# Optimization experiments

Measured on AMD Instinct MI355X. Metric: run time of the kernel, lower is better.

Reference implementation:

```python
import jax, jax.numpy as jnp
import numpy as np

B, PATCH, S, D, LAYERS, TOP_K, N_HEADS = 32, 196, 77, 512, 2, 16, 8


def setup_inputs() -> dict:
    key = jax.random.key(0)
    ks = jax.random.split(key, 16)
    d, L = D, LAYERS
    attn_std = d ** -0.5
    proj_std = (d ** -0.5) * ((2 * L) ** -0.5)
    fc_std = (2 * d) ** -0.5
    scale = d ** -0.5
    f = jnp.float32
    return {
        'image_feature': jax.random.normal(ks[0], (B, d), f),
        'image_tokens': jax.random.normal(ks[1], (B, PATCH, d), f),
        'text_feature': jax.random.normal(ks[2], (B, d), f),
        'text_tokens': jax.random.normal(ks[3], (B, S, d), f),
        'atte_mask': jax.random.randint(ks[4], (B, S), 0, 2).astype(jnp.int32),
        'img_cls': scale * jax.random.normal(ks[5], (d,), f),
        'txt_cls': scale * jax.random.normal(ks[6], (d,), f),
        'in_proj_w': attn_std * jax.random.normal(ks[7], (L, 3 * d, d), f),
        'in_proj_b': jnp.zeros((L, 3 * d), f),
        'out_w': proj_std * jax.random.normal(ks[8], (L, d, d), f),
        'out_b': jnp.zeros((L, d), f),
        'ln1_w': jnp.ones((L, d), f), 'ln1_b': jnp.zeros((L, d), f),
        'ln2_w': jnp.ones((L, d), f), 'ln2_b': jnp.zeros((L, d), f),
        'ln3_w': jnp.ones((L, d), f), 'ln3_b': jnp.zeros((L, d), f),
        'fc_w': fc_std * jax.random.normal(ks[9], (L, 4 * d, d), f),
        'fc_b': jnp.zeros((L, 4 * d), f),
        'proj_w': proj_std * jax.random.normal(ks[10], (L, d, 4 * d), f),
        'proj_b': jnp.zeros((L, d), f),
    }


def _ln(x, w, b):
    m = jnp.mean(x, axis=-1, keepdims=True)
    v = jnp.mean((x - m) ** 2, axis=-1, keepdims=True)
    return (x - m) * jax.lax.rsqrt(v + 1e-5) * w + b


def _mha(q, k, wi, bi, wo, bo):
    # q: (N, Lq, d), k: (N, Lk, d)
    N, Lq, d = q.shape
    hd = d // N_HEADS
    qh = (q @ wi[:d].T + bi[:d]).reshape(N, Lq, N_HEADS, hd)
    kh = (k @ wi[d:2 * d].T + bi[d:2 * d]).reshape(N, -1, N_HEADS, hd)
    vh = (k @ wi[2 * d:].T + bi[2 * d:]).reshape(N, -1, N_HEADS, hd)
    att = jax.nn.softmax(jnp.einsum('bqhd,bkhd->bhqk', qh, kh) * (hd ** -0.5), axis=-1)
    o = jnp.einsum('bhqk,bkhd->bqhd', att, vh).reshape(N, Lq, d)
    return o @ wo.T + bo


def _cross_attention(q4, k4, p):
    shape4 = q4.shape
    q = q4.reshape(-1, q4.shape[-2], q4.shape[-1])
    k = k4.reshape(-1, k4.shape[-2], k4.shape[-1])
    for i in range(LAYERS):
        kn = _ln(k, p['ln2_w'][i], p['ln2_b'][i])
        q = q + _mha(_ln(q, p['ln1_w'][i], p['ln1_b'][i]), kn,
                     p['in_proj_w'][i], p['in_proj_b'][i], p['out_w'][i], p['out_b'][i])
        h = _ln(q, p['ln3_w'][i], p['ln3_b'][i]) @ p['fc_w'][i].T + p['fc_b'][i]
        h = h * jax.nn.sigmoid(1.702 * h)  # QuickGELU
        q = q + h @ p['proj_w'][i].T + p['proj_b'][i]
    return q.reshape(shape4)


def _forward(image_feature, image_tokens, text_feature, text_tokens, atte_mask,
             img_cls, txt_cls, p):
    b, patch, d = image_tokens.shape
    s = text_tokens.shape[1]
    img_n = image_tokens / jnp.linalg.norm(image_tokens, axis=-1, keepdims=True)
    txt_n = text_tokens / jnp.linalg.norm(text_tokens, axis=-1, keepdims=True)
    # pairwise token similarities: (b_img, b_txt, patch, s)
    sim = jnp.einsum('ipd,jsd->ijps', img_n, txt_n)
    img_scores = jnp.einsum('ijps,js->ijp', sim, atte_mask.astype(sim.dtype))
    txt_scores = sim.sum(axis=2)  # (b, b, s)
    # top-k; torch scatter+masked_select gathers in ascending index order
    idx_i = jnp.sort(jax.lax.top_k(img_scores, TOP_K)[1], axis=-1)  # (b,b,k)
    idx_t = jnp.sort(jax.lax.top_k(txt_scores, TOP_K)[1], axis=-1)
    img_sel = img_n[jnp.arange(b)[:, None, None], idx_i]  # (b,b,k,d)
    txt_sel = txt_n[jnp.arange(b)[None, :, None], idx_t]  # (b,b,k,d)
    img_feat = jnp.broadcast_to(image_feature[:, None, None, :], (b, b, 1, d))
    txt_feat = jnp.broadcast_to(text_feature[None, :, None, :], (b, b, 1, d))
    img_cls4 = jnp.broadcast_to(img_cls, (b, b, 1, d))
    txt_cls4 = jnp.broadcast_to(txt_cls, (b, b, 1, d))
    final_img = _cross_attention(jnp.concatenate([img_cls4, img_sel], axis=2),
                                 jnp.concatenate([txt_feat, txt_sel], axis=2), p)
    final_txt = _cross_attention(jnp.concatenate([txt_cls4, txt_sel], axis=2),
                                 jnp.concatenate([img_feat, img_sel], axis=2), p)
    return final_img, final_txt


def reference(image_feature, image_tokens, text_feature, text_tokens, atte_mask,
              img_cls, txt_cls, in_proj_w, in_proj_b, out_w, out_b,
              ln1_w, ln1_b, ln2_w, ln2_b, ln3_w, ln3_b,
              fc_w, fc_b, proj_w, proj_b):
    p = dict(in_proj_w=in_proj_w, in_proj_b=in_proj_b, out_w=out_w, out_b=out_b,
             ln1_w=ln1_w, ln1_b=ln1_b, ln2_w=ln2_w, ln2_b=ln2_b,
             ln3_w=ln3_w, ln3_b=ln3_b, fc_w=fc_w, fc_b=fc_b,
             proj_w=proj_w, proj_b=proj_b)
    return _forward(image_feature, image_tokens, text_feature, text_tokens,
                    atte_mask, img_cls, txt_cls, p)
```

## Files before the change

### kernel.cpp

```cpp
#include <hip/hip_runtime.h>
#include <hip/hip_bf16.h>
#include <stdint.h>


typedef __attribute__((ext_vector_type(8))) short short8;
typedef __attribute__((ext_vector_type(4))) float f32x4;

__device__ __forceinline__ float bf2f(short u) {
    return __uint_as_float(((uint32_t)(uint16_t)u) << 16);
}
__device__ __forceinline__ unsigned short f2bf(float f) {
    __hip_bfloat16 h = __float2bfloat16(f);
    return *reinterpret_cast<unsigned short*>(&h);
}
__device__ __forceinline__ void gload16(const void* g, void* l) {
    __builtin_amdgcn_global_load_lds(
        (const __attribute__((address_space(1))) unsigned int*)g,
        (__attribute__((address_space(3))) unsigned int*)l, 16, 0, 0);
}

__global__ __launch_bounds__(256) void k_f2b4(const float* __restrict__ s0,
                                              const float* __restrict__ s1,
                                              const float* __restrict__ s2,
                                              const float* __restrict__ s3,
                                              unsigned short* __restrict__ out) {
    for (int i = blockIdx.x * 256 + threadIdx.x; i < 6291456; i += gridDim.x * 256) {
        float v;
        if (i < 1572864) v = s0[i];
        else if (i < 2097152) v = s1[i - 1572864];
        else if (i < 4194304) v = s2[i - 2097152];
        else v = s3[i - 4194304];
        out[i] = f2bf(v);
    }
}

__global__ __launch_bounds__(256) void k_l2norm(const float* __restrict__ in,
                                                float* __restrict__ out) {
    size_t row = blockIdx.x;
    const float* x = in + row * 512;
    int t = threadIdx.x;
    float a0 = x[t], a1 = x[t + 256];
    float ss = a0 * a0 + a1 * a1;
#pragma unroll
    for (int off = 32; off; off >>= 1) ss += __shfl_xor(ss, off);
    __shared__ float s4[4];
    if ((t & 63) == 0) s4[t >> 6] = ss;
    __syncthreads();
    float tot = s4[0] + s4[1] + s4[2] + s4[3];
    float inv = 1.0f / sqrtf(tot);
    out[row * 512 + t] = a0 * inv;
    out[row * 512 + t + 256] = a1 * inv;
}

__global__ __launch_bounds__(512) void k_colsum(const float* __restrict__ tok,
                                                const int* __restrict__ mask,
                                                float* __restrict__ out, int R) {
    int b = blockIdx.x;
    int d = threadIdx.x;
    float acc = 0.f;
    for (int r = 0; r < R; r++) {
        float m = mask ? (float)mask[b * R + r] : 1.f;
        acc += m * tok[((size_t)b * R + r) * 512 + d];
    }
    out[b * 512 + d] = acc;
}

__global__ __launch_bounds__(256) void k_scores(const float* __restrict__ tok,
                                                const float* __restrict__ vec,
                                                float* __restrict__ out, int R, int swap) {
    int bid = blockIdx.x;
    int i = bid >> 5, j = bid & 31;
    int tb = swap ? j : i;
    int vb = swap ? i : j;
    __shared__ float sv[512];
    for (int t = threadIdx.x; t < 512; t += 256) sv[t] = vec[vb * 512 + t];
    __syncthreads();
    int wv = threadIdx.x >> 6, lane = threadIdx.x & 63;
    for (int r = wv; r < R; r += 4) {
        const float* tr = tok + ((size_t)tb * R + r) * 512;
        float acc = 0.f;
#pragma unroll
        for (int c = 0; c < 8; c++) {
            int d = lane + c * 64;
            acc += tr[d] * sv[d];
        }
#pragma unroll
        for (int off = 32; off; off >>= 1) acc += __shfl_xor(acc, off);
        if (lane == 0) out[(size_t)bid * R + r] = acc;
    }
}

__global__ __launch_bounds__(64) void k_topk(const float* __restrict__ simg,
                                             const float* __restrict__ stxt,
                                             int* __restrict__ idx_i, int* __restrict__ idx_t) {
    int bid = blockIdx.x;
    bool isimg = bid < 1024;
    int ij = isimg ? bid : bid - 1024;
    const float* s = isimg ? simg + (size_t)ij * 196 : stxt + (size_t)ij * 77;
    int n = isimg ? 196 : 77;
    int* out = (isimg ? idx_i : idx_t) + ij * 16;
    int lane = threadIdx.x;
    float v[4];
    int ids[4];
#pragma unroll
    for (int k = 0; k < 4; k++) {
        int id = lane + k * 64;
        ids[k] = id;
        v[k] = (id < n) ? s[id] : -3.0e38f;
    }
    __shared__ int sel[16];
    for (int r = 0; r < 16; r++) {
        float bv = v[0];
        int bi = ids[0];
#pragma unroll
        for (int k = 1; k < 4; k++)
            if (v[k] > bv) { bv = v[k]; bi = ids[k]; }
#pragma unroll
        for (int off = 32; off; off >>= 1) {
            float ov = __shfl_xor(bv, off);
            int oi = __shfl_xor(bi, off);
            if (ov > bv || (ov == bv && oi < bi)) { bv = ov; bi = oi; }
        }
        if (lane == 0) sel[r] = bi;
#pragma unroll
        for (int k = 0; k < 4; k++)
            if (ids[k] == bi) v[k] = -3.0e38f;
    }
    if (lane == 0) {
        for (int a = 1; a < 16; a++) {
            int key = sel[a];
            int b = a - 1;
            while (b >= 0 && sel[b] > key) { sel[b + 1] = sel[b]; b--; }
            sel[b + 1] = key;
        }
        for (int a = 0; a < 16; a++) out[a] = sel[a];
    }
}

__global__ __launch_bounds__(128) void k_gather(const float* __restrict__ img_n,
                                                const float* __restrict__ txt_n,
                                                const float* __restrict__ img_feat,
                                                const float* __restrict__ txt_feat,
                                                const float* __restrict__ img_cls,
                                                const float* __restrict__ txt_cls,
                                                const int* __restrict__ idx_i,
                                                const int* __restrict__ idx_t,
                                                float* __restrict__ q,
                                                unsigned short* __restrict__ k) {
    int rid = blockIdx.x;
    int buf = rid / 34816;
    int rem = rid % 34816;
    int seq = rem / 17, t = rem % 17;
    int c = seq >> 10, ij = seq & 1023, i = ij >> 5, j = ij & 31;
    const float* src;
    if (buf == 0) {
        if (c == 0)
            src = (t == 0) ? img_cls : img_n + ((size_t)i * 196 + idx_i[ij * 16 + t - 1]) * 512;
        else
            src = (t == 0) ? txt_cls : txt_n + ((size_t)j * 77 + idx_t[ij * 16 + t - 1]) * 512;
    } else {
        if (c == 0)
            src = (t == 0) ? (txt_feat + (size_t)j * 512)
                           : txt_n + ((size_t)j * 77 + idx_t[ij * 16 + t - 1]) * 512;
        else
            src = (t == 0) ? (img_feat + (size_t)i * 512)
                           : img_n + ((size_t)i * 196 + idx_i[ij * 16 + t - 1]) * 512;
    }
    float4 v = ((const float4*)src)[threadIdx.x];
    size_t row = (size_t)seq * 17 + t;
    if (buf == 0) {
        ((float4*)(q + row * 512))[threadIdx.x] = v;
    } else {
        ushort4 o;
        o.x = f2bf(v.x); o.y = f2bf(v.y); o.z = f2bf(v.z); o.w = f2bf(v.w);
        ((ushort4*)(k + row * 512))[threadIdx.x] = o;
    }
}

template <int BF>
__global__ __launch_bounds__(256) void k_ln(const void* __restrict__ xv,
                                            const float* __restrict__ w,
                                            const float* __restrict__ b,
                                            unsigned short* __restrict__ out) {
    int wv = threadIdx.x >> 6, lane = threadIdx.x & 63;
    size_t row = (size_t)blockIdx.x * 4 + wv;
    float v[8];
    if (BF) {
        short8 x = *(const short8*)((const short*)xv + row * 512 + lane * 8);
#pragma unroll
        for (int e = 0; e < 8; e++) v[e] = bf2f(x[e]);
    } else {
        const float* xr = (const float*)xv + row * 512 + lane * 8;
        float4 x0 = *(const float4*)xr;
        float4 x1 = *(const float4*)(xr + 4);
        v[0] = x0.x; v[1] = x0.y; v[2] = x0.z; v[3] = x0.w;
        v[4] = x1.x; v[5] = x1.y; v[6] = x1.z; v[7] = x1.w;
    }
    float s = 0.f, qq = 0.f;
#pragma unroll
    for (int e = 0; e < 8; e++) { s += v[e]; qq += v[e] * v[e]; }
#pragma unroll
    for (int off = 32; off; off >>= 1) {
        s += __shfl_xor(s, off);
        qq += __shfl_xor(qq, off);
    }
    float mean = s * (1.f / 512.f);
    float var = qq * (1.f / 512.f) - mean * mean;
    float rs = rsqrtf(var + 1e-5f);
    const float* wr = w + lane * 8;
    const float* br = b + lane * 8;
    float4 w0 = *(const float4*)wr, w1 = *(const float4*)(wr + 4);
    float4 b0 = *(const float4*)br, b1 = *(const float4*)(br + 4);
    float wv8[8] = {w0.x, w0.y, w0.z, w0.w, w1.x, w1.y, w1.z, w1.w};
    float bv8[8] = {b0.x, b0.y, b0.z, b0.w, b1.x, b1.y, b1.z, b1.w};
    short8 res;
#pragma unroll
    for (int e = 0; e < 8; e++)
        res[e] = (short)f2bf((v[e] - mean) * rs * wv8[e] + bv8[e]);
    *(short8*)(out + row * 512 + lane * 8) = res;
}

template <int MODE>
__global__ __launch_bounds__(256) void k_gemm(const unsigned short* __restrict__ A,
                                              const unsigned short* __restrict__ W,
                                              const float* __restrict__ bias,
                                              void* __restrict__ Cv, int K, int ldc, int nxt) {
    __shared__ __align__(16) short sU[2][8192];

    int nwg = gridDim.x;
    int orig = blockIdx.x;
    int q8 = nwg >> 3, r8 = nwg & 7;
    int xcd = orig & 7, base = orig >> 3;
    int swz = (xcd < r8 ? xcd * (q8 + 1) : r8 * (q8 + 1) + (xcd - r8) * q8) + base;
    int tn = swz % nxt, tm = swz / nxt;

    int tid = threadIdx.x;
    int lane = tid & 63;
    int w = tid >> 6;
    int wm = w >> 1, wn = w & 1;
    int r16 = lane & 15, g = lane >> 4;

    int srow = tid >> 2;
    int sgran = tid & 3;
    int gchunk = (sgran ^ ((srow ^ (srow >> 2)) & 3)) * 8;
    const short* gA = (const short*)A + ((size_t)tm * 128 + srow) * K + gchunk;
    const short* gB = (const short*)W + ((size_t)tn * 128 + srow) * K + gchunk;
    int ldst = tid * 8;

    f32x4 acc[4][4] = {};
    int NU = K >> 5;

#define STAGE_UNIT(U, S)                                              \
    do {                                                              \
        size_t ko_ = (size_t)(U) * 32;                                \
        gload16(gA + ko_, &sU[(S)][ldst]);                            \
        gload16(gA + (size_t)64 * K + ko_, &sU[(S)][2048 + ldst]);    \
        gload16(gB + ko_, &sU[(S)][4096 + ldst]);                     \
        gload16(gB + (size_t)64 * K + ko_, &sU[(S)][6144 + ldst]);    \
    } while (0)

    STAGE_UNIT(0, 0);
    STAGE_UNIT(1, 1);

    int s = 0;
    for (int u = 0; u < NU; ++u) {
        if (u + 1 < NU) asm volatile("s_waitcnt vmcnt(4)" ::: "memory");
        else            asm volatile("s_waitcnt vmcnt(0)" ::: "memory");
        __builtin_amdgcn_s_barrier();
        __builtin_amdgcn_sched_barrier(0);

        const short* SA = &sU[s][0];
        const short* SB = &sU[s][4096];
        short8 a[4], b[4];
#pragma unroll
        for (int m = 0; m < 4; m++) {
            int row = wm * 64 + m * 16 + r16;
            a[m] = *(const short8*)&SA[row * 32 + ((g ^ ((row ^ (row >> 2)) & 3)) << 3)];
        }
#pragma unroll
        for (int n = 0; n < 4; n++) {
            int row = wn * 64 + n * 16 + r16;
            b[n] = *(const short8*)&SB[row * 32 + ((g ^ ((row ^ (row >> 2)) & 3)) << 3)];
        }
        __builtin_amdgcn_s_setprio(1);
#pragma unroll
        for (int m = 0; m < 4; m++)
#pragma unroll
            for (int n = 0; n < 4; n++)
                acc[m][n] = __builtin_amdgcn_mfma_f32_16x16x32_bf16(a[m], b[n], acc[m][n], 0, 0, 0);
        __builtin_amdgcn_s_setprio(0);
        __builtin_amdgcn_sched_barrier(0);
        __builtin_amdgcn_s_barrier();
        if (u + 2 < NU) STAGE_UNIT(u + 2, s);
        s ^= 1;
    }
#undef STAGE_UNIT

    if (MODE == 2) {
        size_t rbase = (size_t)tm * 128 + wm * 64 + g * 4;
        size_t cbase = (size_t)tn * 128 + wn * 64 + r16;
#pragma unroll
        for (int m = 0; m < 4; m++)
#pragma unroll
            for (int n = 0; n < 4; n++) {
                size_t col = cbase + n * 16;
                float bv = bias ? bias[col] : 0.f;
#pragma unroll
                for (int r = 0; r < 4; r++) {
                    size_t row = rbase + m * 16 + r;
                    ((float*)Cv)[row * ldc + col] += acc[m][n][r] + bv;
                }
            }
    } else {
        short* sC = &sU[0][0];
        int lrow = wm * 64 + g * 4;
        int lcol = wn * 64 + r16;
#pragma unroll
        for (int n = 0; n < 4; n++) {
            float bv = bias ? bias[(size_t)tn * 128 + lcol + n * 16] : 0.f;
#pragma unroll
            for (int m = 0; m < 4; m++)
#pragma unroll
                for (int r = 0; r < 4; r++) {
                    float val = acc[m][n][r] + bv;
                    if (MODE == 1) val = val / (1.f + __expf(-1.702f * val));
                    sC[(lrow + m * 16 + r) * 128 + lcol + n * 16] = (short)f2bf(val);
                }
        }
        __builtin_amdgcn_s_barrier();
        unsigned short* C = (unsigned short*)Cv;
#pragma unroll
        for (int p = 0; p < 8; p++) {
            int idx = p * 256 + tid;
            int row = idx >> 4;
            int cc = idx & 15;
            *(short8*)(C + ((size_t)tm * 128 + row) * ldc + (size_t)tn * 128 + cc * 8) =
                *(const short8*)&sC[row * 128 + cc * 8];
        }
    }
}

__global__ __launch_bounds__(512) void k_attn(const unsigned short* __restrict__ Qm,
                                              const unsigned short* __restrict__ KVm,
                                              unsigned short* __restrict__ Om) {
    __shared__ __align__(16) short sAll[3 * 17 * 520];
    __shared__ float sP[8 * 17 * 17];
    int seq = blockIdx.x;
    size_t tb = (size_t)seq * 17;
    for (int c = threadIdx.x; c < 3264; c += 512) {
        int mat = c / 1088, rem = c % 1088, row = rem >> 6, ch = rem & 63;
        const short8* src;
        if (mat == 0)
            src = (const short8*)(Qm + (tb + row) * 512 + ch * 8);
        else if (mat == 1)
            src = (const short8*)(KVm + (tb + row) * 1024 + ch * 8);
        else
            src = (const short8*)(KVm + (tb + row) * 1024 + 512 + ch * 8);
        *(short8*)&sAll[mat * (17 * 520) + row * 520 + ch * 8] = *src;
    }
    __syncthreads();
    int h = threadIdx.x >> 6, lane = threadIdx.x & 63;
    const short* sQ = sAll;
    const short* sK = sAll + 17 * 520;
    const short* sV = sAll + 2 * 17 * 520;
    int jj = lane < 17 ? lane : 0;
    for (int i = 0; i < 17; i++) {
        float acc = 0.f;
#pragma unroll
        for (int c = 0; c < 8; c++) {
            short8 q8 = *(const short8*)&sQ[i * 520 + h * 64 + c * 8];
            short8 k8 = *(const short8*)&sK[jj * 520 + h * 64 + c * 8];
#pragma unroll
            for (int e = 0; e < 8; e++) acc += bf2f(q8[e]) * bf2f(k8[e]);
        }
        float sc = (lane < 17) ? acc * 0.125f : -1e30f;
        float m = sc;
#pragma unroll
        for (int off = 32; off; off >>= 1) m = fmaxf(m, __shfl_xor(m, off));
        float p = (lane < 17) ? __expf(sc - m) : 0.f;
        float sum = p;
#pragma unroll
        for (int off = 32; off; off >>= 1) sum += __shfl_xor(sum, off);
        if (lane < 17) sP[(h * 17 + i) * 17 + lane] = p / sum;
    }
    for (int i = 0; i < 17; i++) {
        float o = 0.f;
#pragma unroll
        for (int t = 0; t < 17; t++)
            o += sP[(h * 17 + i) * 17 + t] * bf2f(sV[t * 520 + h * 64 + lane]);
        Om[(tb + i) * 512 + h * 64 + lane] = f2bf(o);
    }
}

extern "C" void kernel_launch(void* const* d_in, const int* in_sizes, int n_in,
                              void* d_out, int out_size, void* d_ws, size_t ws_size,
                              hipStream_t stream) {
    const float* image_feature = (const float*)d_in[0];
    const float* image_tokens = (const float*)d_in[1];
    const float* text_feature = (const float*)d_in[2];
    const float* text_tokens = (const float*)d_in[3];
    const int* atte_mask = (const int*)d_in[4];
    const float* img_cls = (const float*)d_in[5];
    const float* txt_cls = (const float*)d_in[6];
    const float* in_proj_w = (const float*)d_in[7];
    const float* in_proj_b = (const float*)d_in[8];
    const float* out_w = (const float*)d_in[9];
    const float* out_b = (const float*)d_in[10];
    const float* ln1_w = (const float*)d_in[11];
    const float* ln1_b = (const float*)d_in[12];
    const float* ln2_w = (const float*)d_in[13];
    const float* ln2_b = (const float*)d_in[14];
    const float* ln3_w = (const float*)d_in[15];
    const float* ln3_b = (const float*)d_in[16];
    const float* fc_w = (const float*)d_in[17];
    const float* fc_b = (const float*)d_in[18];
    const float* proj_w = (const float*)d_in[19];
    const float* proj_b = (const float*)d_in[20];

    char* ws = (char*)d_ws;
    const size_t OFF_K = 12582912;
    const size_t OFF_CH = OFF_K + 35651584;
    size_t avail = ws_size > OFF_CH ? ws_size - OFF_CH : 0;
    int C = 2048;
    while (C > 256 && (size_t)87040 * C > avail) C >>= 1;
    int nch = 2048 / C;

    unsigned short* wbf = (unsigned short*)ws;
    unsigned short* w_inproj = wbf;
    unsigned short* w_outp = wbf + 1572864;
    unsigned short* w_fc = wbf + 2097152;
    unsigned short* w_proj = wbf + 4194304;
    unsigned short* kstream = (unsigned short*)(ws + OFF_K);
    char* chreg = ws + OFF_CH;
    float* img_n = (float*)(chreg + 0);
    float* txt_n = (float*)(chreg + 12845056);
    float* isum = (float*)(chreg + 17891328);
    float* tmask = (float*)(chreg + 17956864);
    float* simg = (float*)(chreg + 18022400);
    float* stxt = (float*)(chreg + 18825216);
    int* idx_i = (int*)(chreg + 19140608);
    int* idx_t = (int*)(chreg + 19206144);
    unsigned short* qn = (unsigned short*)chreg;
    unsigned short* qkvQ = (unsigned short*)(chreg + (size_t)17408 * C);
    unsigned short* qkvKV = (unsigned short*)(chreg + (size_t)34816 * C);
    unsigned short* atto = (unsigned short*)(chreg + (size_t)69632 * C);
    unsigned short* hbuf = qkvQ;
    float* q = (float*)d_out;

    k_f2b4<<<3072, 256, 0, stream>>>(in_proj_w, out_w, fc_w, proj_w, wbf);

    k_l2norm<<<6272, 256, 0, stream>>>(image_tokens, img_n);
    k_l2norm<<<2464, 256, 0, stream>>>(text_tokens, txt_n);

    k_colsum<<<32, 512, 0, stream>>>(img_n, nullptr, isum, 196);
    k_colsum<<<32, 512, 0, stream>>>(txt_n, atte_mask, tmask, 77);

    k_scores<<<1024, 256, 0, stream>>>(img_n, tmask, simg, 196, 0);
    k_scores<<<1024, 256, 0, stream>>>(txt_n, isum, stxt, 77, 1);
    k_topk<<<2048, 64, 0, stream>>>(simg, stxt, idx_i, idx_t);
    k_gather<<<69632, 128, 0, stream>>>(img_n, txt_n, image_feature, text_feature,
                                        img_cls, txt_cls, idx_i, idx_t, q, kstream);

    for (int ch = 0; ch < nch; ch++) {
        size_t r0 = (size_t)ch * C * 17;
        float* qc = q + r0 * 512;
        const unsigned short* kc = kstream + r0 * 512;
        int rowsC = 17 * C;
        int gmt = rowsC / 128;
        int gln = rowsC / 4;
        for (int l = 0; l < 2; l++) {
            const unsigned short* Wq = w_inproj + (size_t)l * 786432;
            const unsigned short* Wkv = Wq + 262144;
            const float* bq = in_proj_b + l * 1536;
            const float* bkv = bq + 512;
            k_ln<0><<<gln, 256, 0, stream>>>(qc, ln1_w + l * 512, ln1_b + l * 512, qn);
            k_gemm<0><<<gmt * 4, 256, 0, stream>>>(qn, Wq, bq, qkvQ, 512, 512, 4);
            k_ln<1><<<gln, 256, 0, stream>>>(kc, ln2_w + l * 512, ln2_b + l * 512, qn);
            k_gemm<0><<<gmt * 8, 256, 0, stream>>>(qn, Wkv, bkv, qkvKV, 512, 1024, 8);
            k_attn<<<C, 512, 0, stream>>>(qkvQ, qkvKV, atto);
            k_gemm<2><<<gmt * 4, 256, 0, stream>>>(atto, w_outp + (size_t)l * 262144,
                                                   out_b + l * 512, qc, 512, 512, 4);
            k_ln<0><<<gln, 256, 0, stream>>>(qc, ln3_w + l * 512, ln3_b + l * 512, qn);
            k_gemm<1><<<gmt * 16, 256, 0, stream>>>(qn, w_fc + (size_t)l * 1048576,
                                                    fc_b + l * 2048, hbuf, 512, 2048, 16);
            k_gemm<2><<<gmt * 4, 256, 0, stream>>>(hbuf, w_proj + (size_t)l * 1048576,
                                                   proj_b + l * 512, qc, 2048, 512, 4);
        }
    }
}
```

Before: 1.272 ms.

## Fold ln2 affine into KV weights and fuse layer-0 ln1 into gather

The gather kernel now stores the key stream already normalised (no affine), and the ln2 scale is folded into the bf16 KV weights while the ln2 shift is folded into a precomputed effective KV bias. This drops the per-layer ln2 kernel over the key stream. When everything fits in one chunk, the gather also writes layer-0 ln1 output directly, so the first query LayerNorm launch is skipped. The cost is a small extra bias-precompute kernel and more work inside the gather, with slight numeric changes from folding the affine into bf16 weights.

```diff
diff --git a/kernel.cpp b/kernel.cpp
--- a/kernel.cpp
+++ b/kernel.cpp
@@ -23,15 +23,39 @@
                                               const float* __restrict__ s1,
                                               const float* __restrict__ s2,
                                               const float* __restrict__ s3,
+                                              const float* __restrict__ ln2w,
                                               unsigned short* __restrict__ out) {
     for (int i = blockIdx.x * 256 + threadIdx.x; i < 6291456; i += gridDim.x * 256) {
         float v;
-        if (i < 1572864) v = s0[i];
-        else if (i < 2097152) v = s1[i - 1572864];
+        if (i < 1572864) {
+            v = s0[i];
+            int rem = i % 786432;
+            if (rem >= 262144) {
+                int l = i / 786432;
+                v *= ln2w[l * 512 + (i & 511)];
+            }
+        } else if (i < 2097152) v = s1[i - 1572864];
         else if (i < 4194304) v = s2[i - 2097152];
         else v = s3[i - 4194304];
         out[i] = f2bf(v);
     }
+}
+
+__global__ __launch_bounds__(256) void k_bias2(const float* __restrict__ in_proj_w,
+                                               const float* __restrict__ in_proj_b,
+                                               const float* __restrict__ ln2_b,
+                                               float* __restrict__ b2eff) {
+    int gid = blockIdx.x * 4 + (threadIdx.x >> 6);
+    int l = gid >> 10, o = gid & 1023;
+    int lane = threadIdx.x & 63;
+    const float* wr = in_proj_w + ((size_t)l * 1536 + 512 + o) * 512 + lane * 8;
+    const float* b2 = ln2_b + l * 512 + lane * 8;
+    float acc = 0.f;
+#pragma unroll
+    for (int e = 0; e < 8; e++) acc += wr[e] * b2[e];
+#pragma unroll
+    for (int off = 32; off; off >>= 1) acc += __shfl_xor(acc, off);
+    if (lane == 0) b2eff[l * 1024 + o] = acc + in_proj_b[l * 1536 + 512 + o];
 }
 
 __global__ __launch_bounds__(256) void k_l2norm(const float* __restrict__ in,
@@ -137,16 +161,20 @@
     }
 }
 
-__global__ __launch_bounds__(128) void k_gather(const float* __restrict__ img_n,
-                                                const float* __restrict__ txt_n,
-                                                const float* __restrict__ img_feat,
-                                                const float* __restrict__ txt_feat,
-                                                const float* __restrict__ img_cls,
-                                                const float* __restrict__ txt_cls,
-                                                const int* __restrict__ idx_i,
-                                                const int* __restrict__ idx_t,
-                                                float* __restrict__ q,
-                                                unsigned short* __restrict__ k) {
+__global__ __launch_bounds__(64) void k_gather(const float* __restrict__ img_n,
+                                               const float* __restrict__ txt_n,
+                                               const float* __restrict__ img_feat,
+                                               const float* __restrict__ txt_feat,
+                                               const float* __restrict__ img_cls,
+                                               const float* __restrict__ txt_cls,
+                                               const int* __restrict__ idx_i,
+                                               const int* __restrict__ idx_t,
+                                               const float* __restrict__ ln1w0,
+                                               const float* __restrict__ ln1b0,
+                                               float* __restrict__ q,
+                                               unsigned short* __restrict__ kn,
+                                               unsigned short* __restrict__ qn0,
+                                               int fold) {
     int rid = blockIdx.x;
     int buf = rid / 34816;
     int rem = rid % 34816;
@@ -166,36 +194,52 @@
             src = (t == 0) ? (img_feat + (size_t)i * 512)
                            : img_n + ((size_t)i * 196 + idx_i[ij * 16 + t - 1]) * 512;
     }
-    float4 v = ((const float4*)src)[threadIdx.x];
+    int lane = threadIdx.x;
+    const float* sp = src + lane * 8;
+    float4 x0 = *(const float4*)sp;
+    float4 x1 = *(const float4*)(sp + 4);
+    float v[8] = {x0.x, x0.y, x0.z, x0.w, x1.x, x1.y, x1.z, x1.w};
+    float s = 0.f, qq = 0.f;
+#pragma unroll
+    for (int e = 0; e < 8; e++) { s += v[e]; qq += v[e] * v[e]; }
+#pragma unroll
+    for (int off = 32; off; off >>= 1) {
+        s += __shfl_xor(s, off);
+        qq += __shfl_xor(qq, off);
+    }
+    float mean = s * (1.f / 512.f);
+    float var = qq * (1.f / 512.f) - mean * mean;
+    float rs = rsqrtf(var + 1e-5f);
     size_t row = (size_t)seq * 17 + t;
     if (buf == 0) {
-        ((float4*)(q + row * 512))[threadIdx.x] = v;
+        float* qd = q + row * 512 + lane * 8;
+        *(float4*)qd = x0;
+        *(float4*)(qd + 4) = x1;
+        if (fold) {
+            short8 o;
+#pragma unroll
+            for (int e = 0; e < 8; e++)
+                o[e] = (short)f2bf((v[e] - mean) * rs * ln1w0[lane * 8 + e] + ln1b0[lane * 8 + e]);
+            *(short8*)(qn0 + row * 512 + lane * 8) = o;
+        }
     } else {
-        ushort4 o;
-        o.x = f2bf(v.x); o.y = f2bf(v.y); o.z = f2bf(v.z); o.w = f2bf(v.w);
-        ((ushort4*)(k + row * 512))[threadIdx.x] = o;
-    }
-}
-
-template <int BF>
-__global__ __launch_bounds__(256) void k_ln(const void* __restrict__ xv,
+        short8 o;
+#pragma unroll
+        for (int e = 0; e < 8; e++) o[e] = (short)f2bf((v[e] - mean) * rs);
+        *(short8*)(kn + row * 512 + lane * 8) = o;
+    }
+}
+
+__global__ __launch_bounds__(256) void k_ln(const float* __restrict__ xv,
                                             const float* __restrict__ w,
                                             const float* __restrict__ b,
                                             unsigned short* __restrict__ out) {
     int wv = threadIdx.x >> 6, lane = threadIdx.x & 63;
     size_t row = (size_t)blockIdx.x * 4 + wv;
-    float v[8];
-    if (BF) {
-        short8 x = *(const short8*)((const short*)xv + row * 512 + lane * 8);
-#pragma unroll
-        for (int e = 0; e < 8; e++) v[e] = bf2f(x[e]);
-    } else {
-        const float* xr = (const float*)xv + row * 512 + lane * 8;
-        float4 x0 = *(const float4*)xr;
-        float4 x1 = *(const float4*)(xr + 4);
-        v[0] = x0.x; v[1] = x0.y; v[2] = x0.z; v[3] = x0.w;
-        v[4] = x1.x; v[5] = x1.y; v[6] = x1.z; v[7] = x1.w;
-    }
+    const float* xr = xv + row * 512 + lane * 8;
+    float4 x0 = *(const float4*)xr;
+    float4 x1 = *(const float4*)(xr + 4);
+    float v[8] = {x0.x, x0.y, x0.z, x0.w, x1.x, x1.y, x1.z, x1.w};
     float s = 0.f, qq = 0.f;
 #pragma unroll
     for (int e = 0; e < 8; e++) { s += v[e]; qq += v[e] * v[e]; }
@@ -419,7 +463,8 @@
 
     char* ws = (char*)d_ws;
     const size_t OFF_K = 12582912;
-    const size_t OFF_CH = OFF_K + 35651584;
+    const size_t OFF_B2 = OFF_K + 35651584;
+    const size_t OFF_CH = OFF_B2 + 8192;
     size_t avail = ws_size > OFF_CH ? ws_size - OFF_CH : 0;
     int C = 2048;
     while (C > 256 && (size_t)87040 * C > avail) C >>= 1;
@@ -431,6 +476,7 @@
     unsigned short* w_fc = wbf + 2097152;
     unsigned short* w_proj = wbf + 4194304;
     unsigned short* kstream = (unsigned short*)(ws + OFF_K);
+    float* b2eff = (float*)(ws + OFF_B2);
     char* chreg = ws + OFF_CH;
     float* img_n = (float*)(chreg + 0);
     float* txt_n = (float*)(chreg + 12845056);
@@ -445,9 +491,12 @@
     unsigned short* qkvKV = (unsigned short*)(chreg + (size_t)34816 * C);
     unsigned short* atto = (unsigned short*)(chreg + (size_t)69632 * C);
     unsigned short* hbuf = qkvQ;
+    unsigned short* qn0 = atto;
     float* q = (float*)d_out;
-
-    k_f2b4<<<3072, 256, 0, stream>>>(in_proj_w, out_w, fc_w, proj_w, wbf);
+    int fold = (nch == 1) ? 1 : 0;
+
+    k_f2b4<<<3072, 256, 0, stream>>>(in_proj_w, out_w, fc_w, proj_w, ln2_w, wbf);
+    k_bias2<<<512, 256, 0, stream>>>(in_proj_w, in_proj_b, ln2_b, b2eff);
 
     k_l2norm<<<6272, 256, 0, stream>>>(image_tokens, img_n);
     k_l2norm<<<2464, 256, 0, stream>>>(text_tokens, txt_n);
@@ -458,8 +507,9 @@
     k_scores<<<1024, 256, 0, stream>>>(img_n, tmask, simg, 196, 0);
     k_scores<<<1024, 256, 0, stream>>>(txt_n, isum, stxt, 77, 1);
     k_topk<<<2048, 64, 0, stream>>>(simg, stxt, idx_i, idx_t);
-    k_gather<<<69632, 128, 0, stream>>>(img_n, txt_n, image_feature, text_feature,
-                                        img_cls, txt_cls, idx_i, idx_t, q, kstream);
+    k_gather<<<69632, 64, 0, stream>>>(img_n, txt_n, image_feature, text_feature,
+                                       img_cls, txt_cls, idx_i, idx_t,
+                                       ln1_w, ln1_b, q, kstream, qn0, fold);
 
     for (int ch = 0; ch < nch; ch++) {
         size_t r0 = (size_t)ch * C * 17;
@@ -472,15 +522,20 @@
             const unsigned short* Wq = w_inproj + (size_t)l * 786432;
             const unsigned short* Wkv = Wq + 262144;
             const float* bq = in_proj_b + l * 1536;
-            const float* bkv = bq + 512;
-            k_ln<0><<<gln, 256, 0, stream>>>(qc, ln1_w + l * 512, ln1_b + l * 512, qn);
-            k_gemm<0><<<gmt * 4, 256, 0, stream>>>(qn, Wq, bq, qkvQ, 512, 512, 4);
-            k_ln<1><<<gln, 256, 0, stream>>>(kc, ln2_w + l * 512, ln2_b + l * 512, qn);
-            k_gemm<0><<<gmt * 8, 256, 0, stream>>>(qn, Wkv, bkv, qkvKV, 512, 1024, 8);
+            const unsigned short* Aq;
+            if (l == 0 && fold) {
+                Aq = qn0;
+            } else {
+                k_ln<<<gln, 256, 0, stream>>>(qc, ln1_w + l * 512, ln1_b + l * 512, qn);
+                Aq = qn;
+            }
+            k_gemm<0><<<gmt * 4, 256, 0, stream>>>(Aq, Wq, bq, qkvQ, 512, 512, 4);
+            k_gemm<0><<<gmt * 8, 256, 0, stream>>>(kc, Wkv, b2eff + l * 1024, qkvKV,
+                                                   512, 1024, 8);
             k_attn<<<C, 512, 0, stream>>>(qkvQ, qkvKV, atto);
             k_gemm<2><<<gmt * 4, 256, 0, stream>>>(atto, w_outp + (size_t)l * 262144,
                                                    out_b + l * 512, qc, 512, 512, 4);
-            k_ln<0><<<gln, 256, 0, stream>>>(qc, ln3_w + l * 512, ln3_b + l * 512, qn);
+            k_ln<<<gln, 256, 0, stream>>>(qc, ln3_w + l * 512, ln3_b + l * 512, qn);
             k_gemm<1><<<gmt * 16, 256, 0, stream>>>(qn, w_fc + (size_t)l * 1048576,
                                                     fc_b + l * 2048, hbuf, 512, 2048, 16);
             k_gemm<2><<<gmt * 4, 256, 0, stream>>>(hbuf, w_proj + (size_t)l * 1048576,
```

New measurement: 1.238 ms. 2.7% less time.
